# Optimization experiments

Hardware: AMD Instinct MI355X
Metric: run time of the kernel (lower is better)

Reference implementation:

```python
import jax, jax.numpy as jnp
import numpy as np

J = 3
J_H = 5
C_IN = 128
C_OUT = 128
N0, N1, N2 = 1024, 3072, 2048
DENSITY = 0.01
W_SCALE = 0.02  # keeps P^(2^(J_h-1)) @ x @ W magnitudes reasonable in fp32


def _sym_sparse(key, n, density):
    kv, km = jax.random.split(key)
    mask = jax.random.uniform(km, (n, n)) < density
    a = jnp.where(mask, jax.random.normal(kv, (n, n)), 0.0)
    return jnp.triu(a) + jnp.triu(a, 1).T  # symmetric sparse 'Laplacian'


def _sparse(kv, km, shape, density):
    mask = jax.random.uniform(km, shape) < density
    return jnp.where(mask, jax.random.normal(kv, shape), 0.0)


def setup_inputs() -> dict:
    key = jax.random.key(0)
    ks = jax.random.split(key, 24)
    z0 = jax.random.normal(ks[0], (N0, C_IN), jnp.float32)
    z1 = jax.random.normal(ks[1], (N1, C_IN), jnp.float32)
    z2 = jax.random.normal(ks[2], (N2, C_IN), jnp.float32)
    L0 = _sym_sparse(ks[3], N0, 0.02)
    L1_d = _sym_sparse(ks[4], N1, DENSITY)
    L1_u = _sym_sparse(ks[5], N1, DENSITY)
    L2 = _sym_sparse(ks[6], N2, DENSITY)
    B1 = _sparse(ks[7], ks[8], (N0, N1), DENSITY)
    B2 = _sparse(ks[9], ks[10], (N1, N2), DENSITY)
    W_d = jax.random.normal(ks[11], (J, C_IN, C_OUT)) * W_SCALE
    W_u = jax.random.normal(ks[12], (J, C_IN, C_OUT)) * W_SCALE
    W_h = jax.random.normal(ks[13], (C_IN, C_OUT)) * W_SCALE
    W_b1 = jax.random.normal(ks[14], (J, C_IN, C_OUT)) * W_SCALE
    W_b2 = jax.random.normal(ks[15], (J, C_IN, C_OUT)) * W_SCALE
    attn_d_w = jax.random.normal(ks[16], (1, 2 * C_IN)) * W_SCALE
    attn_d_b = jax.random.normal(ks[17], (1,)) * W_SCALE
    attn_u_w = jax.random.normal(ks[18], (1, 2 * C_IN)) * W_SCALE
    attn_u_b = jax.random.normal(ks[19], (1,)) * W_SCALE
    return dict(z0=z0, z1=z1, z2=z2, L0=L0, L1_d=L1_d, L1_u=L1_u, L2=L2,
                B1=B1, B2=B2, W_d=W_d, W_u=W_u, W_h=W_h, W_b1=W_b1, W_b2=W_b2,
                attn_d_w=attn_d_w, attn_d_b=attn_d_b,
                attn_u_w=attn_u_w, attn_u_b=attn_u_b)


def _attention(x, n, w, b, src, dst):
    # gather edge endpoints -> tiny MLP -> sigmoid -> symmetric scatter
    a = jnp.concatenate([x[src], x[dst]], axis=-1)      # [E, 2C]
    s = jax.nn.sigmoid(a @ w.T + b)[:, 0]               # [E]
    return jnp.zeros((n, n), x.dtype).at[src, dst].set(s).at[dst, src].set(s)


def _harmonic(L, x, W_h):
    lmax = jnp.linalg.eigvalsh(L)[-1]
    # torch does lambda_max.item() -> constant w.r.t. grads
    eps = jax.lax.stop_gradient(jnp.where(lmax > 0, 1.0 / lmax, 0.1))
    P = jnp.eye(L.shape[0], dtype=x.dtype) - eps * L
    for _ in range(J_H - 1):
        P = P @ P                                        # P^(2^(J_h-1))
    return P @ x @ W_h


def reference(z0, z1, z2, L0, L1_d, L1_u, L2, B1, B2,
              W_d, W_u, W_h, W_b1, W_b2,
              attn_d_w, attn_d_b, attn_u_w, attn_u_b):
    # nonzero patterns of the Laplacians (constants, computed on host)
    src_d, dst_d = np.nonzero(np.asarray(jax.device_get(L1_d)))
    src_u, dst_u = np.nonzero(np.asarray(jax.device_get(L1_u)))
    L1d_attn = _attention(z1, N1, attn_d_w, attn_d_b,
                          jnp.asarray(src_d), jnp.asarray(dst_d))
    L1u_attn = _attention(z1, N1, attn_u_w, attn_u_b,
                          jnp.asarray(src_u), jnp.asarray(dst_u))
    # sum_j (A @ z) @ W[j] == (A @ z) @ W.sum(0)
    Wd_s, Wu_s = W_d.sum(0), W_u.sum(0)
    Wb1_s, Wb2_s = W_b1.sum(0), W_b2.sum(0)

    z0_out = (L0 @ z0) @ Wd_s + (B1 @ z1) @ Wb1_s + _harmonic(L0, z0, W_h)
    z0_out = jax.nn.relu(z0_out)

    z1_out = ((L1d_attn @ z1) @ Wd_s + (L1u_attn @ z1) @ Wu_s
              + (B1.T @ z0) @ Wb1_s + (B2 @ z2) @ Wb2_s
              + _harmonic(L1_d + L1_u, z1, W_h))
    z1_out = jax.nn.relu(z1_out)

    z2_out = (L2 @ z2) @ Wu_s + (B2.T @ z1) @ Wb2_s + _harmonic(L2, z2, W_h)
    z2_out = jax.nn.relu(z2_out)
    return (z0_out, z1_out, z2_out)
```

## Files before the change

kernel.cpp:

```cpp
#include <hip/hip_runtime.h>
#include <string.h>

constexpr int M_LZ = 48;

constexpr int CAP_L0 = 26240, CAP_L1 = 118016, CAP_L2 = 52480, CAP_B1 = 39360, CAP_B2 = 78720;
constexpr int CB_L0 = 0;
constexpr int CB_L1D = CB_L0 + CAP_L0;
constexpr int CB_L1U = CB_L1D + CAP_L1;
constexpr int CB_L2  = CB_L1U + CAP_L1;
constexpr int CB_B1  = CB_L2 + CAP_L2;
constexpr int CB_B2  = CB_B1 + CAP_B1;
constexpr int CAP_TOT= CB_B2 + CAP_B2;
constexpr int CB_B1T = CAP_TOT;
constexpr int CB_B2T = CB_B1T + CAP_B1;
constexpr int CAP_TOT2 = CB_B2T + CAP_B2;

constexpr int P_L0=0, P_L1D=1025, P_L1U=4098, P_L2=7171, P_B1=9220, P_B2=10245;
constexpr int P_B1T=13320, P_B2T=16393;
constexpr int C_L0=0, C_L1D=1024, C_L1U=4096, C_L2=7168, C_B1=9216, C_B2=10240;
constexpr int C_B1T=13312, C_B2T=16384;

constexpr size_t HBUF  = (size_t)6144*128;

constexpr size_t W_CNT = 0;
constexpr size_t W_PTR = 18432;
constexpr size_t W_CUR = W_PTR + 18444;
constexpr size_t W_CIDX= W_CUR + 5120;
constexpr size_t W_VAL = W_CIDX + CAP_TOT2;
constexpr size_t W_V0  = W_VAL + CAP_TOT2;
constexpr size_t W_PK  = W_V0 + 6144;
constexpr size_t W_TT  = W_PK + (size_t)64*6144*4;
constexpr size_t W_EPS = W_TT + 6144;
constexpr size_t W_UV  = W_EPS + 128;
constexpr size_t W_H   = W_UV + 4*3072;
constexpr size_t W_SCAT= W_H + 15*HBUF;
constexpr size_t S0_OFF= 0;
constexpr size_t S1_OFF= (size_t)1024*384;
constexpr size_t S2_OFF= S1_OFF + (size_t)3072*640;
constexpr size_t SCAT_TOT = S2_OFF + (size_t)2048*384;
constexpr size_t W_WCAT= W_SCAT + SCAT_TOT;
constexpr size_t WC0=0, WC1=(size_t)384*128, WC2=WC1+(size_t)640*128;
constexpr size_t W_SLOT= W_WCAT + (size_t)1408*128;
constexpr size_t W_FLG = W_SLOT + 1048576;
constexpr size_t W_REL = W_FLG + 65536;

__device__ __forceinline__ float wredf(float v){
  #pragma unroll
  for(int o=32;o;o>>=1) v += __shfl_xor(v,o,64);
  return v;
}
__device__ __forceinline__ int wredi(int v){
  #pragma unroll
  for(int o=32;o;o>>=1) v += __shfl_xor(v,o,64);
  return v;
}
__device__ __forceinline__ void red4x2(float4& a0, float4& a1){
  #pragma unroll
  for (int o=16;o<=32;o<<=1){
    a0.x+=__shfl_xor(a0.x,o,64); a0.y+=__shfl_xor(a0.y,o,64);
    a0.z+=__shfl_xor(a0.z,o,64); a0.w+=__shfl_xor(a0.w,o,64);
    a1.x+=__shfl_xor(a1.x,o,64); a1.y+=__shfl_xor(a1.y,o,64);
    a1.z+=__shfl_xor(a1.z,o,64); a1.w+=__shfl_xor(a1.w,o,64);
  }
}
__device__ __forceinline__ float v0hash(int i, float invs){
  unsigned uu=(unsigned)i*2654435761u; uu^=uu>>16; uu*=2246822519u; uu^=uu>>13;
  return (uu&1)?invs:-invs;
}

__device__ __forceinline__ float ldc(const float* p){
  return __hip_atomic_load(p, __ATOMIC_RELAXED, __HIP_MEMORY_SCOPE_AGENT);
}
__device__ __forceinline__ float2 ldc2(const float* p){
  unsigned long long u = __hip_atomic_load((const unsigned long long*)p,
                          __ATOMIC_RELAXED, __HIP_MEMORY_SCOPE_AGENT);
  float2 r; memcpy(&r,&u,8); return r;
}
__device__ __forceinline__ void stc(float* p, float v){
  __hip_atomic_store(p, v, __ATOMIC_RELAXED, __HIP_MEMORY_SCOPE_AGENT);
}
__device__ __forceinline__ void stc2(float* p, float2 v){
  unsigned long long u; memcpy(&u,&v,8);
  __hip_atomic_store((unsigned long long*)p, u, __ATOMIC_RELAXED, __HIP_MEMORY_SCOPE_AGENT);
}
__device__ __forceinline__ int ldci(const int* p){
  return __hip_atomic_load(p, __ATOMIC_RELAXED, __HIP_MEMORY_SCOPE_AGENT);
}
__device__ __forceinline__ void stci(int* p, int v){
  __hip_atomic_store(p, v, __ATOMIC_RELAXED, __HIP_MEMORY_SCOPE_AGENT);
}

__device__ __forceinline__ void barg(float* ws, int* leafs, int b, int lbase, int Ng,
                                     bool chk, int lidx, int ph){
  const int t = threadIdx.x;
  int* flg = (int*)ws + W_FLG;
  __builtin_amdgcn_s_waitcnt(0);
  __syncthreads();
  if (t==0) stci(flg + (size_t)b*32, ph+1);
  if (chk){
    for (int s=t; s<Ng; s+=256){
      const int* f = flg + (size_t)(lbase+s)*32;
      while (ldci(f) < ph+1) __builtin_amdgcn_s_sleep(1);
    }
    __syncthreads();
    if (t==0){
      #pragma unroll
      for (int i=0;i<16;i++) stci(leafs + (size_t)i*32, ph+1);
    }
    __syncthreads();
  } else {
    if (t==0){
      const int* rl = leafs + (size_t)(lidx&15)*32;
      while (ldci(rl) < ph+1) __builtin_amdgcn_s_sleep(1);
    }
    __syncthreads();
  }
}

__device__ __forceinline__ void bar_lz(float* ws, int b, int grp, int lbase, int Lg,
                                       bool chk, int lb, int ph, int j,
                                       float* shr, float* redm,
                                       float& a_o, float& g_o, float& ib_o){
  const int t = threadIdx.x, lane = t&63, wvv = t>>6;
  __builtin_amdgcn_s_waitcnt(0);
  __syncthreads();
  if (t==0){
    float A0=redm[0]+redm[1]+redm[2]+redm[3];
    float G0=redm[4]+redm[5]+redm[6]+redm[7];
    float N0=redm[8]+redm[9]+redm[10]+redm[11];
    float* sl = ws + W_SLOT + ((size_t)j*2048 + b)*8;
    stc2(sl+2, make_float2(A0,G0)); stc(sl+4, N0);
    __builtin_amdgcn_s_waitcnt(0);
    stci((int*)sl, ph+1);
  }
  if (chk){
    float pa=0.f, pg=0.f, pn=0.f;
    for (int s=t; s<Lg; s+=256){
      const float* sl = ws + W_SLOT + ((size_t)j*2048 + lbase+s)*8;
      while (ldci((const int*)sl) < ph+1) __builtin_amdgcn_s_sleep(1);
      float2 ag = ldc2(sl+2); float nn = ldc(sl+4);
      pa+=ag.x; pg+=ag.y; pn+=nn;
    }
    pa=wredf(pa); pg=wredf(pg); pn=wredf(pn);
    if (lane==0){ shr[0*4+wvv]=pa; shr[1*4+wvv]=pg; shr[2*4+wvv]=pn; }
    __syncthreads();
    if (t==0){
      float a=shr[0]+shr[1]+shr[2]+shr[3];
      float g=shr[4]+shr[5]+shr[6]+shr[7];
      float n=shr[8]+shr[9]+shr[10]+shr[11];
      float ib = 1.f/sqrtf(fmaxf(n - a*a - g*g, 1e-20f));
      float* TT = ws + W_TT + (size_t)(grp*64 + j)*32;
      stc2(TT, make_float2(a,g)); stc(TT+2, n);
      #pragma unroll
      for (int i=0;i<16;i++){
        float* lf = ws + W_REL + (size_t)(grp*16+i)*32;
        stc2(lf+2, make_float2(a,g)); stc(lf+4, ib);
      }
      __builtin_amdgcn_s_waitcnt(0);
      #pragma unroll
      for (int i=0;i<16;i++)
        stci((int*)(ws + W_REL) + (size_t)(grp*16+i)*32, ph+1);
      shr[0]=a; shr[1]=g; shr[2]=ib;
    }
    __syncthreads();
  } else {
    if (t==0){
      const float* lf = ws + W_REL + (size_t)(grp*16 + (lb&15))*32;
      while (ldci((const int*)lf) < ph+1) __builtin_amdgcn_s_sleep(1);
      float2 ag = ldc2(lf+2); float ib = ldc(lf+4);
      shr[0]=ag.x; shr[1]=ag.y; shr[2]=ib;
    }
    __syncthreads();
  }
  a_o = shr[0]; g_o = shr[1]; ib_o = shr[2];
}

__global__ void k_wprep(const float* Wd,const float* Wu,const float* Wh,
                        const float* Wb1,const float* Wb2, float* ws){
  int t = blockIdx.x*256 + threadIdx.x;
  if (t >= 16384) return;
  int* wsi = (int*)ws;
  if (t < 5120) wsi[W_CNT + 13312 + t] = 0;
  if (t < 5120) wsi[W_CUR + t] = 0;
  for (int i=t; i<65536+2048; i+=16384) wsi[W_FLG+i] = 0;
  for (int i=t; i<131072; i+=16384) wsi[W_SLOT + (size_t)i*8] = 0;
  float sd = Wd[t]  + Wd[16384+t]  + Wd[32768+t];
  float su = Wu[t]  + Wu[16384+t]  + Wu[32768+t];
  float s1 = Wb1[t] + Wb1[16384+t] + Wb1[32768+t];
  float s2 = Wb2[t] + Wb2[16384+t] + Wb2[32768+t];
  float wh = Wh[t];
  float* W0 = ws + W_WCAT + WC0;
  float* W1 = ws + W_WCAT + WC1;
  float* W2 = ws + W_WCAT + WC2;
  W0[t]=sd; W0[16384+t]=s1; W0[32768+t]=wh;
  W1[t]=sd; W1[16384+t]=su; W1[32768+t]=s1; W1[49152+t]=s2; W1[65536+t]=wh;
  W2[t]=su; W2[16384+t]=s2; W2[32768+t]=wh;
}

__device__ __forceinline__ void mat_meta(int wid, const float* L0,const float* L1d,const float* L1u,
    const float* L2,const float* B1,const float* B2,
    const float*& M,int& ncol,int& lrow,int& co,int& po,int& cb,int& cap,int& tco){
  if (wid < 1024){ M=L0;  ncol=1024; lrow=wid;        co=C_L0;  po=P_L0;  cb=CB_L0;  cap=CAP_L0; tco=-1; }
  else if (wid < 4096){ M=L1d; ncol=3072; lrow=wid-1024;  co=C_L1D; po=P_L1D; cb=CB_L1D; cap=CAP_L1; tco=-1; }
  else if (wid < 7168){ M=L1u; ncol=3072; lrow=wid-4096;  co=C_L1U; po=P_L1U; cb=CB_L1U; cap=CAP_L1; tco=-1; }
  else if (wid < 9216){ M=L2;  ncol=2048; lrow=wid-7168;  co=C_L2;  po=P_L2;  cb=CB_L2;  cap=CAP_L2; tco=-1; }
  else if (wid < 10240){ M=B1; ncol=3072; lrow=wid-9216;  co=C_B1;  po=P_B1;  cb=CB_B1;  cap=CAP_B1; tco=C_B1T; }
  else { M=B2; ncol=2048; lrow=wid-10240; co=C_B2;  po=P_B2;  cb=CB_B2;  cap=CAP_B2; tco=C_B2T; }
}

__global__ void k_count(const float* L0,const float* L1d,const float* L1u,const float* L2,
                        const float* B1,const float* B2,int* cnt){
  int wid = blockIdx.x*4 + (threadIdx.x>>6);
  int lane = threadIdx.x & 63;
  if (wid >= 13312) return;
  const float* M; int ncol,lrow,co,po,cb,cap,tco;
  mat_meta(wid,L0,L1d,L1u,L2,B1,B2,M,ncol,lrow,co,po,cb,cap,tco);
  const float4* row4 = (const float4*)(M + (size_t)lrow*ncol);
  int c = 0;
  for (int j0=0; j0<ncol; j0+=256){
    float4 v = row4[(j0>>2)+lane];
    int n0=v.x!=0.f, n1=v.y!=0.f, n2=v.z!=0.f, n3=v.w!=0.f;
    c += n0+n1+n2+n3;
    if (tco>=0){
      int jb = j0 + lane*4;
      if (n0) atomicAdd(cnt+tco+jb,   1);
      if (n1) atomicAdd(cnt+tco+jb+1, 1);
      if (n2) atomicAdd(cnt+tco+jb+2, 1);
      if (n3) atomicAdd(cnt+tco+jb+3, 1);
    }
  }
  c = wredi(c);
  if (lane==0) cnt[co+lrow] = c;
}

__global__ void k_prefix(const int* cnt, int* ptr, int* cur){
  __shared__ int lds[257];
  const int rows[8]={1024,3072,3072,2048,1024,3072,3072,2048};
  const int cofs[8]={C_L0,C_L1D,C_L1U,C_L2,C_B1,C_B2,C_B1T,C_B2T};
  const int pofs[8]={P_L0,P_L1D,P_L1U,P_L2,P_B1,P_B2,P_B1T,P_B2T};
  int b=blockIdx.x, t=threadIdx.x;
  int R=rows[b]; const int* c=cnt+cofs[b]; int* p=ptr+pofs[b];
  int* cc = (b==6)? cur : (b==7)? cur+3072 : nullptr;
  int chunk=(R+255)/256;
  int lo=t*chunk, hi=min(R,lo+chunk);
  int s=0;
  for(int i=lo;i<hi;i++) s+=c[i];
  lds[t]=s; __syncthreads();
  if(t==0){ int run=0; for(int i=0;i<256;i++){int x=lds[i];lds[i]=run;run+=x;} lds[256]=run; }
  __syncthreads();
  int run=lds[t];
  for(int i=lo;i<hi;i++){ p[i]=run; if(cc) cc[i]=run; run+=c[i]; }
  if(t==0) p[R]=lds[256];
}

__global__ void k_fill(const float* L0,const float* L1d,const float* L1u,const float* L2,
                       const float* B1,const float* B2,const int* ptr,int* cidx,float* val){
  int wid = blockIdx.x*4 + (threadIdx.x>>6);
  int lane = threadIdx.x & 63;
  if (wid >= 13312) return;
  const float* M; int ncol,lrow,co,po,cb,cap,tco;
  mat_meta(wid,L0,L1d,L1u,L2,B1,B2,M,ncol,lrow,co,po,cb,cap,tco);
  const float4* row4 = (const float4*)(M + (size_t)lrow*ncol);
  int base = ptr[po+lrow];
  int run = 0;
  for (int j0=0; j0<ncol; j0+=256){
    float4 v = row4[(j0>>2)+lane];
    int n0=v.x!=0.f, n1=v.y!=0.f, n2=v.z!=0.f, n3=v.w!=0.f;
    int local = n0+n1+n2+n3;
    int incl = local;
    #pragma unroll
    for (int o=1;o<64;o<<=1){
      int tmp = __shfl_up(incl,o,64);
      if (lane>=o) incl += tmp;
    }
    int tot = __shfl(incl,63,64);
    int pos = base + run + incl - local;
    int jb = j0 + lane*4;
    if (n0){ if(pos<cap){cidx[cb+pos]=jb;   val[cb+pos]=v.x;} pos++; }
    if (n1){ if(pos<cap){cidx[cb+pos]=jb+1; val[cb+pos]=v.y;} pos++; }
    if (n2){ if(pos<cap){cidx[cb+pos]=jb+2; val[cb+pos]=v.z;} pos++; }
    if (n3){ if(pos<cap){cidx[cb+pos]=jb+3; val[cb+pos]=v.w;} pos++; }
    run += tot;
  }
}

__global__ void k_fillT(float* ws){
  int wid = blockIdx.x*4 + (threadIdx.x>>6);
  int lane = threadIdx.x & 63;
  if (wid >= 4096) return;
  int* wsi=(int*)ws;
  const int* ptr=wsi+W_PTR; int* cidx=wsi+W_CIDX; float* val=ws+W_VAL;
  int* cur=wsi+W_CUR;
  if (wid < 1024){
    int r=wid;
    int e=ptr[P_B1+r+1];
    for(int k=ptr[P_B1+r]+lane;k<e;k+=64){
      int c=cidx[CB_B1+k]; float v=val[CB_B1+k];
      int pos=atomicAdd(cur+c,1);
      cidx[CB_B1T+pos]=r; val[CB_B1T+pos]=v;
    }
  } else {
    int r=wid-1024;
    int e=ptr[P_B2+r+1];
    for(int k=ptr[P_B2+r]+lane;k<e;k+=64){
      int c=cidx[CB_B2+k]; float v=val[CB_B2+k];
      int pos=atomicAdd(cur+3072+c,1);
      cidx[CB_B2T+pos]=r; val[CB_B2T+pos]=v;
    }
  }
}

__global__ __launch_bounds__(256,8) void k_solve(float* ws,
    const float* z0,const float* z1,const float* z2,
    const float* adw,const float* adb,const float* auw,const float* aub,
    float* out){
  const int b = blockIdx.x, t = threadIdx.x;
  const int wv = t>>6, lane = t&63;
  const int sg = lane>>4, chn = lane&15;
  const int* wsi=(const int*)ws;
  const int* ptr=wsi+W_PTR; const int* cidx=wsi+W_CIDX; const float* val=ws+W_VAL;

  __shared__ float smem[2616];
  float* Sl  = smem;
  float* Wl  = smem + 544;
  float* TTa = smem;
  float* TTb = smem + 64;
  float* redm= smem + 2592;
  float* shr = smem + 2604;

  int* grel = (int*)ws + W_REL + 48*32;
  int* krel = (int*)ws + W_SLOT + 63*2048*8;

  if (b < 768){
    int g, gbase, nb;
    if (b<128){ g=0; gbase=0;   nb=0;    }
    else if (b<512){ g=1; gbase=128; nb=1024; }
    else { g=2; gbase=512; nb=4096; }
    const int lb = b - gbase;
    const int Lg = (g==0)?128:(g==1)?384:256;
    const bool chk = (lb==0);
    const float invsg = (g==0)?0.03125f:(g==1)?0.0180421959f:0.0220970869f;
    const int hw = lane>>5, hl = lane&31;
    const int p  = lb*8 + wv*2 + hw;
    const int gp = nb + p;
    float a=0.f, gmm=0.f, ib=1.f;
    float vp_m1=0.f, vp_m2=0.f, wp_m1=0.f;
    for (int j=0;j<M_LZ;j++){
      float wp=0.f;
      if (j==0){
        #define GZ(PP,CBB) { const int* rp=ptr+PP; int e=rp[p+1]; \
          for (int k=rp[p]+hl;k<e;k+=32){ wp += val[CBB+k]*v0hash(nb+cidx[CBB+k], invsg); } }
        if (g==0){ GZ(P_L0,CB_L0) }
        else if (g==1){ GZ(P_L1D,CB_L1D) GZ(P_L1U,CB_L1U) }
        else { GZ(P_L2,CB_L2) }
        #undef GZ
      } else {
        const float4* pk = (const float4*)(ws + W_PK) + (size_t)(j-1)*6144 + nb;
        #define GP(PP,CBB) { const int* rp=ptr+PP; int e=rp[p+1]; \
          for (int k=rp[p]+hl;k<e;k+=32){ float v=val[CBB+k]; float4 pq=pk[cidx[CBB+k]]; \
            wp += v*((pq.x - a*pq.y - gmm*pq.z)*ib); } }
        if (g==0){ GP(P_L0,CB_L0) }
        else if (g==1){ GP(P_L1D,CB_L1D) GP(P_L1U,CB_L1U) }
        else { GP(P_L2,CB_L2) }
        #undef GP
      }
      #pragma unroll
      for (int o=16;o;o>>=1) wp += __shfl_xor(wp,o,64);
      float rA=0.f, rG=0.f, rN=0.f;
      if (hl==0){
        float vp;
        if (j==0) vp = v0hash(gp, invsg);
        else      vp = (wp_m1 - a*vp_m1 - gmm*vp_m2)*ib;
        float* pkw = ws + W_PK + ((size_t)j*6144 + gp)*4;
        stc2(pkw, make_float2(wp, vp)); stc(pkw+2, vp_m1);
        rA = vp*wp; rG = vp_m1*wp; rN = wp*wp;
        vp_m2 = vp_m1; vp_m1 = vp; wp_m1 = wp;
      }
      rA += __shfl_xor(rA,32,64); rG += __shfl_xor(rG,32,64); rN += __shfl_xor(rN,32,64);
      if (lane==0){ redm[0*4+wv]=rA; redm[1*4+wv]=rG; redm[2*4+wv]=rN; }
      bar_lz(ws, b, g, gbase, Lg, chk, lb, 1+j, j, shr, redm, a, gmm, ib);
    }
    if (chk && t<64){
      int i = t;
      double lo=1e300, hi=-1e300;
      if (i<M_LZ){
        const float* TT = ws + W_TT + (size_t)(g*64 + i)*32;
        float aa=TT[0], gg=TT[1], nn=TT[2];
        TTa[i]=aa; TTb[i]=sqrtf(fmaxf(nn-aa*aa-gg*gg,1e-20f));
      }
      if (i<M_LZ){
        double r=(i? fabs((double)TTb[i-1]):0.0) + (i<M_LZ-1? fabs((double)TTb[i]):0.0);
        lo=(double)TTa[i]-r; hi=(double)TTa[i]+r;
      }
      #pragma unroll
      for(int o=32;o;o>>=1){ lo=fmin(lo,__shfl_xor(lo,o,64)); hi=fmax(hi,__shfl_xor(hi,o,64)); }
      lo -= 1.0; hi += 1.0;
      for (int round=0; round<4; round++){
        double x = lo + (hi-lo)*(double)(i+1)/65.0;
        double d = 1.0; int cnt2=0;
        for (int k2=0;k2<M_LZ;k2++){
          double bi = k2? (double)TTb[k2-1] : 0.0;
          d = ((double)TTa[k2]-x) - bi*bi/d;
          if (d==0.0) d = -1e-300;
          if (d<0.0) cnt2++;
        }
        double nlo = (cnt2< M_LZ)? x : -1e300;
        double nhi = (cnt2==M_LZ)? x :  1e300;
        #pragma unroll
        for(int o=32;o;o>>=1){ nlo=fmax(nlo,__shfl_xor(nlo,o,64)); nhi=fmin(nhi,__shfl_xor(nhi,o,64)); }
        if (nlo>-1e299) lo=nlo;
        if (nhi< 1e299) hi=nhi;
      }
      double lam = 0.5*(lo+hi);
      if (i==0) stc(ws+W_EPS+(size_t)g*32, (lam>0.0)? (float)(1.0/lam) : 0.1f);
    }
  } else {
    const int kb = b - 768;
    const int vw = kb*4 + wv;
    if (vw < 3072){
      float2 x  = ((const float2*)(z1+(size_t)vw*128))[lane];
      float2 a0 = ((const float2*)adw)[lane];
      float2 a1 = ((const float2*)adw)[64+lane];
      float2 b0 = ((const float2*)auw)[lane];
      float2 b1 = ((const float2*)auw)[64+lane];
      float ud=x.x*a0.x+x.y*a0.y, vd=x.x*a1.x+x.y*a1.y;
      float uu=x.x*b0.x+x.y*b0.y, vu=x.x*b1.x+x.y*b1.y;
      ud=wredf(ud); vd=wredf(vd); uu=wredf(uu); vu=wredf(vu);
      if(lane==0){ stc(ws+W_UV+vw,ud); stc(ws+W_UV+3072+vw,vd);
                   stc(ws+W_UV+6144+vw,uu); stc(ws+W_UV+9216+vw,vu); }
    }
    int cgP, nbP, lrP; float e0P;
    if (vw < 3072){ cgP=1; nbP=1024; lrP=vw;      e0P=(1.f/28.f); }
    else          { cgP=2; nbP=4096; lrP=vw-3072; e0P=0.0625f;    }
    const bool has2 = (vw >= 4096);
    const int lr2 = vw - 4096;
    for (int k2=1; k2<=16; k2++){
      const float* ybase = ws + W_H + (size_t)(k2>=2? k2-2:0)*HBUF;
      #define KG2(PP,CBB,NBV,ZZV,LRV) { const int* rp=ptr+PP; int e=rp[(LRV)+1]; \
        for (int kk=rp[LRV]+sg; kk<e; kk+=4){ \
          float v=val[CBB+kk]; int q=cidx[CBB+kk]; \
          const float* sr = (k2==1)? (ZZV)+(size_t)q*128 : ybase+(size_t)((NBV)+q)*128; \
          float4 x0=((const float4*)sr)[chn*2], x1=((const float4*)sr)[chn*2+1]; \
          a0.x+=v*x0.x; a0.y+=v*x0.y; a0.z+=v*x0.z; a0.w+=v*x0.w; \
          a1.x+=v*x1.x; a1.y+=v*x1.y; a1.z+=v*x1.z; a1.w+=v*x1.w; \
        } }
      #define KWRITE(CGV,LRV,GRV,E0V) if (lane<16){ \
          float* dst; \
          if (k2<16) dst = ws + W_H + (size_t)(k2-1)*HBUF + (size_t)(GRV)*128; \
          else { \
            if ((CGV)==0)      dst = ws+W_SCAT+S0_OFF+256 + (size_t)(LRV)*384; \
            else if ((CGV)==1) dst = ws+W_SCAT+S1_OFF+512 + (size_t)(LRV)*640; \
            else               dst = ws+W_SCAT+S2_OFF+256 + (size_t)(LRV)*384; \
          } \
          stc2(dst+chn*8,   make_float2((E0V)*a0.x, (E0V)*a0.y)); \
          stc2(dst+chn*8+2, make_float2((E0V)*a0.z, (E0V)*a0.w)); \
          stc2(dst+chn*8+4, make_float2((E0V)*a1.x, (E0V)*a1.y)); \
          stc2(dst+chn*8+6, make_float2((E0V)*a1.z, (E0V)*a1.w)); }
      {
        float4 a0={0.f,0.f,0.f,0.f}, a1={0.f,0.f,0.f,0.f};
        if (cgP==1){ KG2(P_L1D,CB_L1D,1024,z1,lrP) KG2(P_L1U,CB_L1U,1024,z1,lrP) }
        else { KG2(P_L2,CB_L2,4096,z2,lrP) }
        red4x2(a0,a1);
        KWRITE(cgP, lrP, nbP+lrP, e0P)
      }
      if (has2){
        float4 a0={0.f,0.f,0.f,0.f}, a1={0.f,0.f,0.f,0.f};
        KG2(P_L0,CB_L0,0,z0,lr2)
        red4x2(a0,a1);
        KWRITE(0, lr2, lr2, 0.0625f)
      }
      #undef KG2
      #undef KWRITE
      if (k2<16) barg(ws, krel, b, 768, 1280, b==768, kb, k2);
    }
    for (int wid2 = kb*4+wv; wid2 < 18432; wid2 += 5120){
      int task,p2;
      if(wid2<1024){task=0;p2=wid2;}
      else if(wid2<2048){task=1;p2=wid2-1024;}
      else if(wid2<5120){task=2;p2=wid2-2048;}
      else if(wid2<8192){task=3;p2=wid2-5120;}
      else if(wid2<11264){task=4;p2=wid2-8192;}
      else if(wid2<13312){task=5;p2=wid2-11264;}
      else if(wid2<16384){task=6;p2=wid2-13312;}
      else {task=7;p2=wid2-16384;}
      const float* in; const int* rp; int cb2; float* outp; int ostride;
      int mode=0; float Vp=0.f, bb=0.f; const float* U=nullptr;
      switch(task){
        case 0: rp=ptr+P_L0;  cb2=CB_L0;  in=z0; outp=ws+W_SCAT+S0_OFF+0;   ostride=384; break;
        case 1: rp=ptr+P_B1;  cb2=CB_B1;  in=z1; outp=ws+W_SCAT+S0_OFF+128; ostride=384; break;
        case 2: rp=ptr+P_L1D; cb2=CB_L1D; in=z1; outp=ws+W_SCAT+S1_OFF+0;   ostride=640;
                mode=1; U=ws+W_UV; Vp=ws[W_UV+3072+p2]; bb=adb[0]; break;
        case 3: rp=ptr+P_L1U; cb2=CB_L1U; in=z1; outp=ws+W_SCAT+S1_OFF+128; ostride=640;
                mode=1; U=ws+W_UV+6144; Vp=ws[W_UV+9216+p2]; bb=aub[0]; break;
        case 4: rp=ptr+P_B2;  cb2=CB_B2;  in=z2; outp=ws+W_SCAT+S1_OFF+384; ostride=640; break;
        case 5: rp=ptr+P_L2;  cb2=CB_L2;  in=z2; outp=ws+W_SCAT+S2_OFF+0;   ostride=384; break;
        case 6: rp=ptr+P_B1T; cb2=CB_B1T; in=z0; outp=ws+W_SCAT+S1_OFF+256; ostride=640; break;
        default:rp=ptr+P_B2T; cb2=CB_B2T; in=z1; outp=ws+W_SCAT+S2_OFF+128; ostride=384; break;
      }
      float4 a0={0.f,0.f,0.f,0.f}, a1={0.f,0.f,0.f,0.f};
      int e=rp[p2+1];
      for (int k=rp[p2]+sg; k<e; k+=4){
        int q = cidx[cb2+k];
        float v;
        if (mode) v = 1.0f/(1.0f+__expf(-(U[q]+Vp+bb)));
        else v = val[cb2+k];
        const float* sr = in + (size_t)q*128;
        float4 x0 = ((const float4*)sr)[chn*2];
        float4 x1 = ((const float4*)sr)[chn*2+1];
        a0.x+=v*x0.x; a0.y+=v*x0.y; a0.z+=v*x0.z; a0.w+=v*x0.w;
        a1.x+=v*x1.x; a1.y+=v*x1.y; a1.z+=v*x1.z; a1.w+=v*x1.w;
      }
      red4x2(a0, a1);
      if (sg==0){
        float* dst = outp + (size_t)p2*ostride;
        stc2(dst+chn*8,   make_float2(a0.x,a0.y));
        stc2(dst+chn*8+2, make_float2(a0.z,a0.w));
        stc2(dst+chn*8+4, make_float2(a1.x,a1.y));
        stc2(dst+chn*8+6, make_float2(a1.z,a1.w));
      }
    }
  }

  barg(ws, grel, b, 0, 2048, b==1, b, 30);

  { int r = b*4+wv;
    if (r < 6144){
      int cg = (r<1024)?0:(r<4096)?1:2;
      int lr = r - ((cg==0)?0:(cg==1)?1024:4096);
      const float* zz = (cg==0)?z0:(cg==1)?z1:z2;
      float lam0 = (cg==1)?28.f:16.f;
      float eps  = ws[W_EPS+(size_t)cg*32];
      float rr = eps*lam0;
      float* hc;
      if (cg==0)      hc = ws+W_SCAT+S0_OFF+256 + (size_t)lr*384;
      else if (cg==1) hc = ws+W_SCAT+S1_OFF+512 + (size_t)lr*640;
      else            hc = ws+W_SCAT+S2_OFF+256 + (size_t)lr*384;
      const float BIN[17] = {1.f,16.f,120.f,560.f,1820.f,4368.f,8008.f,11440.f,12870.f,
                             11440.f,8008.f,4368.f,1820.f,560.f,120.f,16.f,1.f};
      float2 acc = ((const float2*)(zz + (size_t)lr*128))[lane];
      float rk = 1.f;
      #pragma unroll
      for (int k2=1;k2<=15;k2++){
        rk *= -rr;
        float2 y = ((const float2*)(ws + W_H + (size_t)(k2-1)*HBUF + (size_t)r*128))[lane];
        float c = BIN[k2]*rk;
        acc.x += c*y.x; acc.y += c*y.y;
      }
      rk *= -rr;
      float2 y16 = ((const float2*)hc)[lane];
      acc.x += rk*y16.x; acc.y += rk*y16.y;
      stc2(hc + (size_t)lane*2, acc);
    }
  }
  barg(ws, grel, b, 0, 2048, b==1, b, 31);

  if (b < 192){
    const float* S; const float* W; float* outp; int K; int blk;
    if (b<32){       S=ws+W_SCAT+S0_OFF; W=ws+W_WCAT+WC0; outp=out;        K=384; blk=b; }
    else if (b<128){ S=ws+W_SCAT+S1_OFF; W=ws+W_WCAT+WC1; outp=out+131072; K=640; blk=b-32; }
    else {           S=ws+W_SCAT+S2_OFF; W=ws+W_WCAT+WC2; outp=out+524288; K=384; blk=b-128; }
    int r0=blk*32;
    int ty=t>>5, tx=t&31;
    float acc[4][4]={};
    for (int k0=0; k0<K; k0+=16){
      {
        int r=t>>3, kq=(t&7)*2;
        const float* src=S+(size_t)(r0+r)*K + k0+kq;
        Sl[r*17+kq]=src[0]; Sl[r*17+kq+1]=src[1];
      }
      {
        int kk=t>>4, cq=(t&15)*8;
        const float* src=W+(size_t)(k0+kk)*128+cq;
        #pragma unroll
        for(int i=0;i<8;i++) Wl[kk*128+cq+i]=src[i];
      }
      __syncthreads();
      #pragma unroll
      for(int k=0;k<16;k++){
        float sv[4], wvv2[4];
        #pragma unroll
        for(int i=0;i<4;i++) sv[i]=Sl[(ty*4+i)*17+k];
        #pragma unroll
        for(int i=0;i<4;i++) wvv2[i]=Wl[k*128+tx+32*i];
        #pragma unroll
        for(int a2=0;a2<4;a2++)
          #pragma unroll
          for(int b2=0;b2<4;b2++) acc[a2][b2]+=sv[a2]*wvv2[b2];
      }
      __syncthreads();
    }
    #pragma unroll
    for(int a2=0;a2<4;a2++)
      #pragma unroll
      for(int b2=0;b2<4;b2++){
        int r=r0+ty*4+a2, col=tx+32*b2;
        outp[(size_t)r*128+col]=fmaxf(acc[a2][b2],0.f);
      }
  }
}

extern "C" void kernel_launch(void* const* d_in, const int* in_sizes, int n_in,
                              void* d_out, int out_size, void* d_ws, size_t ws_size,
                              hipStream_t stream){
  const float* z0 =(const float*)d_in[0];
  const float* z1 =(const float*)d_in[1];
  const float* z2 =(const float*)d_in[2];
  const float* L0 =(const float*)d_in[3];
  const float* L1d=(const float*)d_in[4];
  const float* L1u=(const float*)d_in[5];
  const float* L2 =(const float*)d_in[6];
  const float* B1 =(const float*)d_in[7];
  const float* B2 =(const float*)d_in[8];
  const float* Wd =(const float*)d_in[9];
  const float* Wu =(const float*)d_in[10];
  const float* Wh =(const float*)d_in[11];
  const float* Wb1=(const float*)d_in[12];
  const float* Wb2=(const float*)d_in[13];
  const float* adw=(const float*)d_in[14];
  const float* adb=(const float*)d_in[15];
  const float* auw=(const float*)d_in[16];
  const float* aub=(const float*)d_in[17];
  float* ws=(float*)d_ws;
  int* wsi=(int*)d_ws;
  float* out=(float*)d_out;

  hipLaunchKernelGGL(k_wprep, dim3(64), dim3(256), 0, stream, Wd,Wu,Wh,Wb1,Wb2,ws);
  hipLaunchKernelGGL(k_count, dim3(3328), dim3(256), 0, stream, L0,L1d,L1u,L2,B1,B2, wsi+W_CNT);
  hipLaunchKernelGGL(k_prefix, dim3(8), dim3(256), 0, stream, wsi+W_CNT, wsi+W_PTR, wsi+W_CUR);
  hipLaunchKernelGGL(k_fill, dim3(3328), dim3(256), 0, stream, L0,L1d,L1u,L2,B1,B2, wsi+W_PTR, wsi+W_CIDX, ws+W_VAL);
  hipLaunchKernelGGL(k_fillT, dim3(1024), dim3(256), 0, stream, ws);
  hipLaunchKernelGGL(k_solve, dim3(2048), dim3(256), 0, stream,
                     ws, z0, z1, z2, adw, adb, auw, aub, out);
}
```

Before: 780.1 us.

## Fuse CSR build kernels into persistent solve kernel with grid barriers

The count, prefix, fill and transpose-fill kernels are folded into the single persistent solve kernel, separated by grid-wide barriers. The transpose fill is moved into the blocks that previously only waited during the Lanczos phase, so it overlaps that work. The intent is to remove four kernel launches and their inter-kernel gaps. In exchange the stages depend on software grid barriers, and many loads and stores become cache-bypassing so that data written before a barrier is visible across blocks.

```diff
diff --git a/kernel.cpp b/kernel.cpp
--- a/kernel.cpp
+++ b/kernel.cpp
@@ -180,8 +180,8 @@
   int t = blockIdx.x*256 + threadIdx.x;
   if (t >= 16384) return;
   int* wsi = (int*)ws;
-  if (t < 5120) wsi[W_CNT + 13312 + t] = 0;
-  if (t < 5120) wsi[W_CUR + t] = 0;
+  if (t < 5120) stci(wsi + W_CNT + 13312 + t, 0);
+  if (t < 5120) stci(wsi + W_CUR + t, 0);
   for (int i=t; i<65536+2048; i+=16384) wsi[W_FLG+i] = 0;
   for (int i=t; i<131072; i+=16384) wsi[W_SLOT + (size_t)i*8] = 0;
   float sd = Wd[t]  + Wd[16384+t]  + Wd[32768+t];
@@ -208,117 +208,18 @@
   else { M=B2; ncol=2048; lrow=wid-10240; co=C_B2;  po=P_B2;  cb=CB_B2;  cap=CAP_B2; tco=C_B2T; }
 }
 
-__global__ void k_count(const float* L0,const float* L1d,const float* L1u,const float* L2,
-                        const float* B1,const float* B2,int* cnt){
-  int wid = blockIdx.x*4 + (threadIdx.x>>6);
-  int lane = threadIdx.x & 63;
-  if (wid >= 13312) return;
-  const float* M; int ncol,lrow,co,po,cb,cap,tco;
-  mat_meta(wid,L0,L1d,L1u,L2,B1,B2,M,ncol,lrow,co,po,cb,cap,tco);
-  const float4* row4 = (const float4*)(M + (size_t)lrow*ncol);
-  int c = 0;
-  for (int j0=0; j0<ncol; j0+=256){
-    float4 v = row4[(j0>>2)+lane];
-    int n0=v.x!=0.f, n1=v.y!=0.f, n2=v.z!=0.f, n3=v.w!=0.f;
-    c += n0+n1+n2+n3;
-    if (tco>=0){
-      int jb = j0 + lane*4;
-      if (n0) atomicAdd(cnt+tco+jb,   1);
-      if (n1) atomicAdd(cnt+tco+jb+1, 1);
-      if (n2) atomicAdd(cnt+tco+jb+2, 1);
-      if (n3) atomicAdd(cnt+tco+jb+3, 1);
-    }
-  }
-  c = wredi(c);
-  if (lane==0) cnt[co+lrow] = c;
-}
-
-__global__ void k_prefix(const int* cnt, int* ptr, int* cur){
-  __shared__ int lds[257];
-  const int rows[8]={1024,3072,3072,2048,1024,3072,3072,2048};
-  const int cofs[8]={C_L0,C_L1D,C_L1U,C_L2,C_B1,C_B2,C_B1T,C_B2T};
-  const int pofs[8]={P_L0,P_L1D,P_L1U,P_L2,P_B1,P_B2,P_B1T,P_B2T};
-  int b=blockIdx.x, t=threadIdx.x;
-  int R=rows[b]; const int* c=cnt+cofs[b]; int* p=ptr+pofs[b];
-  int* cc = (b==6)? cur : (b==7)? cur+3072 : nullptr;
-  int chunk=(R+255)/256;
-  int lo=t*chunk, hi=min(R,lo+chunk);
-  int s=0;
-  for(int i=lo;i<hi;i++) s+=c[i];
-  lds[t]=s; __syncthreads();
-  if(t==0){ int run=0; for(int i=0;i<256;i++){int x=lds[i];lds[i]=run;run+=x;} lds[256]=run; }
-  __syncthreads();
-  int run=lds[t];
-  for(int i=lo;i<hi;i++){ p[i]=run; if(cc) cc[i]=run; run+=c[i]; }
-  if(t==0) p[R]=lds[256];
-}
-
-__global__ void k_fill(const float* L0,const float* L1d,const float* L1u,const float* L2,
-                       const float* B1,const float* B2,const int* ptr,int* cidx,float* val){
-  int wid = blockIdx.x*4 + (threadIdx.x>>6);
-  int lane = threadIdx.x & 63;
-  if (wid >= 13312) return;
-  const float* M; int ncol,lrow,co,po,cb,cap,tco;
-  mat_meta(wid,L0,L1d,L1u,L2,B1,B2,M,ncol,lrow,co,po,cb,cap,tco);
-  const float4* row4 = (const float4*)(M + (size_t)lrow*ncol);
-  int base = ptr[po+lrow];
-  int run = 0;
-  for (int j0=0; j0<ncol; j0+=256){
-    float4 v = row4[(j0>>2)+lane];
-    int n0=v.x!=0.f, n1=v.y!=0.f, n2=v.z!=0.f, n3=v.w!=0.f;
-    int local = n0+n1+n2+n3;
-    int incl = local;
-    #pragma unroll
-    for (int o=1;o<64;o<<=1){
-      int tmp = __shfl_up(incl,o,64);
-      if (lane>=o) incl += tmp;
-    }
-    int tot = __shfl(incl,63,64);
-    int pos = base + run + incl - local;
-    int jb = j0 + lane*4;
-    if (n0){ if(pos<cap){cidx[cb+pos]=jb;   val[cb+pos]=v.x;} pos++; }
-    if (n1){ if(pos<cap){cidx[cb+pos]=jb+1; val[cb+pos]=v.y;} pos++; }
-    if (n2){ if(pos<cap){cidx[cb+pos]=jb+2; val[cb+pos]=v.z;} pos++; }
-    if (n3){ if(pos<cap){cidx[cb+pos]=jb+3; val[cb+pos]=v.w;} pos++; }
-    run += tot;
-  }
-}
-
-__global__ void k_fillT(float* ws){
-  int wid = blockIdx.x*4 + (threadIdx.x>>6);
-  int lane = threadIdx.x & 63;
-  if (wid >= 4096) return;
-  int* wsi=(int*)ws;
-  const int* ptr=wsi+W_PTR; int* cidx=wsi+W_CIDX; float* val=ws+W_VAL;
-  int* cur=wsi+W_CUR;
-  if (wid < 1024){
-    int r=wid;
-    int e=ptr[P_B1+r+1];
-    for(int k=ptr[P_B1+r]+lane;k<e;k+=64){
-      int c=cidx[CB_B1+k]; float v=val[CB_B1+k];
-      int pos=atomicAdd(cur+c,1);
-      cidx[CB_B1T+pos]=r; val[CB_B1T+pos]=v;
-    }
-  } else {
-    int r=wid-1024;
-    int e=ptr[P_B2+r+1];
-    for(int k=ptr[P_B2+r]+lane;k<e;k+=64){
-      int c=cidx[CB_B2+k]; float v=val[CB_B2+k];
-      int pos=atomicAdd(cur+3072+c,1);
-      cidx[CB_B2T+pos]=r; val[CB_B2T+pos]=v;
-    }
-  }
-}
-
-__global__ __launch_bounds__(256,8) void k_solve(float* ws,
+__global__ __launch_bounds__(256,8) void k_all(float* ws,
     const float* z0,const float* z1,const float* z2,
+    const float* L0,const float* L1d,const float* L1u,
+    const float* L2,const float* B1,const float* B2,
     const float* adw,const float* adb,const float* auw,const float* aub,
     float* out){
   const int b = blockIdx.x, t = threadIdx.x;
   const int wv = t>>6, lane = t&63;
   const int sg = lane>>4, chn = lane&15;
-  const int* wsi=(const int*)ws;
-  const int* ptr=wsi+W_PTR; const int* cidx=wsi+W_CIDX; const float* val=ws+W_VAL;
+  int* wsi=(int*)ws;
+  int* ptrm=wsi+W_PTR; int* cnm=wsi+W_CNT;
+  int* cidxm=wsi+W_CIDX; float* valm=ws+W_VAL;
 
   __shared__ float smem[2616];
   float* Sl  = smem;
@@ -330,6 +231,78 @@
 
   int* grel = (int*)ws + W_REL + 48*32;
   int* krel = (int*)ws + W_SLOT + 63*2048*8;
+
+  for (int wid = b*4+wv; wid < 13312; wid += 8192){
+    const float* M; int ncol,lrow,co,po,cb,cap,tco;
+    mat_meta(wid,L0,L1d,L1u,L2,B1,B2,M,ncol,lrow,co,po,cb,cap,tco);
+    const float4* row4 = (const float4*)(M + (size_t)lrow*ncol);
+    int c = 0;
+    for (int j0=0; j0<ncol; j0+=256){
+      float4 v = row4[(j0>>2)+lane];
+      int n0=v.x!=0.f, n1=v.y!=0.f, n2=v.z!=0.f, n3=v.w!=0.f;
+      c += n0+n1+n2+n3;
+      if (tco>=0){
+        int jb = j0 + lane*4;
+        if (n0) atomicAdd(cnm+tco+jb,   1);
+        if (n1) atomicAdd(cnm+tco+jb+1, 1);
+        if (n2) atomicAdd(cnm+tco+jb+2, 1);
+        if (n3) atomicAdd(cnm+tco+jb+3, 1);
+      }
+    }
+    c = wredi(c);
+    if (lane==0) stci(cnm+co+lrow, c);
+  }
+  barg(ws, grel, b, 0, 2048, b==0, b, 0);
+
+  if (b < 8){
+    int* lds = (int*)smem;
+    const int rows[8]={1024,3072,3072,2048,1024,3072,3072,2048};
+    const int cofs[8]={C_L0,C_L1D,C_L1U,C_L2,C_B1,C_B2,C_B1T,C_B2T};
+    const int pofs[8]={P_L0,P_L1D,P_L1U,P_L2,P_B1,P_B2,P_B1T,P_B2T};
+    int R=rows[b]; const int* c=cnm+cofs[b]; int* p=ptrm+pofs[b];
+    int* cc = (b==6)? (wsi+W_CUR) : (b==7)? (wsi+W_CUR+3072) : nullptr;
+    int chunk=(R+255)/256;
+    int lo=t*chunk, hi=min(R,lo+chunk);
+    int s=0;
+    for(int i=lo;i<hi;i++) s+=ldci(c+i);
+    lds[t]=(float)0, ((int*)lds)[t]=s; __syncthreads();
+    if(t==0){ int run=0; for(int i=0;i<256;i++){int x=((int*)lds)[i];((int*)lds)[i]=run;run+=x;} ((int*)lds)[256]=run; }
+    __syncthreads();
+    int run=((int*)lds)[t];
+    for(int i=lo;i<hi;i++){ stci(p+i, run); if(cc) stci(cc+i, run); run+=ldci(c+i); }
+    if(t==0) stci(p+R, ((int*)lds)[256]);
+  }
+  barg(ws, grel, b, 0, 2048, b==0, b, 1);
+
+  for (int wid = b*4+wv; wid < 13312; wid += 8192){
+    const float* M; int ncol,lrow,co,po,cb,cap,tco;
+    mat_meta(wid,L0,L1d,L1u,L2,B1,B2,M,ncol,lrow,co,po,cb,cap,tco);
+    const float4* row4 = (const float4*)(M + (size_t)lrow*ncol);
+    int base = ldci(ptrm+po+lrow);
+    int run = 0;
+    for (int j0=0; j0<ncol; j0+=256){
+      float4 v = row4[(j0>>2)+lane];
+      int n0=v.x!=0.f, n1=v.y!=0.f, n2=v.z!=0.f, n3=v.w!=0.f;
+      int local = n0+n1+n2+n3;
+      int incl = local;
+      #pragma unroll
+      for (int o=1;o<64;o<<=1){
+        int tmp = __shfl_up(incl,o,64);
+        if (lane>=o) incl += tmp;
+      }
+      int tot = __shfl(incl,63,64);
+      int pos = base + run + incl - local;
+      int jb = j0 + lane*4;
+      if (n0){ if(pos<cap){stci(cidxm+cb+pos,jb);   stc(valm+cb+pos,v.x);} pos++; }
+      if (n1){ if(pos<cap){stci(cidxm+cb+pos,jb+1); stc(valm+cb+pos,v.y);} pos++; }
+      if (n2){ if(pos<cap){stci(cidxm+cb+pos,jb+2); stc(valm+cb+pos,v.z);} pos++; }
+      if (n3){ if(pos<cap){stci(cidxm+cb+pos,jb+3); stc(valm+cb+pos,v.w);} pos++; }
+      run += tot;
+    }
+  }
+  barg(ws, grel, b, 0, 2048, b==0, b, 2);
+
+  const int* ptr=ptrm; const int* cidx=cidxm; const float* val=valm;
 
   if (b < 768){
     int g, gbase, nb;
@@ -385,7 +358,7 @@
       double lo=1e300, hi=-1e300;
       if (i<M_LZ){
         const float* TT = ws + W_TT + (size_t)(g*64 + i)*32;
-        float aa=TT[0], gg=TT[1], nn=TT[2];
+        float aa=ldc(TT), gg=ldc(TT+1), nn=ldc(TT+2);
         TTa[i]=aa; TTb[i]=sqrtf(fmaxf(nn-aa*aa-gg*gg,1e-20f));
       }
       if (i<M_LZ){
@@ -415,6 +388,28 @@
       if (i==0) stc(ws+W_EPS+(size_t)g*32, (lam>0.0)? (float)(1.0/lam) : 0.1f);
     }
   } else {
+    { int widT = (b-768)*4+wv;
+      if (widT < 4096){
+        int* cur=wsi+W_CUR;
+        if (widT < 1024){
+          int r=widT;
+          int s0=ldci(ptr+P_B1+r); int e=ldci(ptr+P_B1+r+1);
+          for(int k=s0+lane;k<e;k+=64){
+            int c=ldci(cidx+CB_B1+k); float v=ldc(val+CB_B1+k);
+            int pos=atomicAdd(cur+c,1);
+            stci(cidxm+CB_B1T+pos,r); stc(valm+CB_B1T+pos,v);
+          }
+        } else {
+          int r=widT-1024;
+          int s0=ldci(ptr+P_B2+r); int e=ldci(ptr+P_B2+r+1);
+          for(int k=s0+lane;k<e;k+=64){
+            int c=ldci(cidx+CB_B2+k); float v=ldc(val+CB_B2+k);
+            int pos=atomicAdd(cur+3072+c,1);
+            stci(cidxm+CB_B2T+pos,r); stc(valm+CB_B2T+pos,v);
+          }
+        }
+      }
+    }
     const int kb = b - 768;
     const int vw = kb*4 + wv;
     if (vw < 3072){
@@ -471,7 +466,7 @@
       }
       #undef KG2
       #undef KWRITE
-      if (k2<16) barg(ws, krel, b, 768, 1280, b==768, kb, k2);
+      if (k2<16) barg(ws, krel, b, 768, 1280, b==768, kb, k2+3);
     }
     for (int wid2 = kb*4+wv; wid2 < 18432; wid2 += 5120){
       int task,p2;
@@ -489,9 +484,9 @@
         case 0: rp=ptr+P_L0;  cb2=CB_L0;  in=z0; outp=ws+W_SCAT+S0_OFF+0;   ostride=384; break;
         case 1: rp=ptr+P_B1;  cb2=CB_B1;  in=z1; outp=ws+W_SCAT+S0_OFF+128; ostride=384; break;
         case 2: rp=ptr+P_L1D; cb2=CB_L1D; in=z1; outp=ws+W_SCAT+S1_OFF+0;   ostride=640;
-                mode=1; U=ws+W_UV; Vp=ws[W_UV+3072+p2]; bb=adb[0]; break;
+                mode=1; U=ws+W_UV; Vp=ldc(ws+W_UV+3072+p2); bb=adb[0]; break;
         case 3: rp=ptr+P_L1U; cb2=CB_L1U; in=z1; outp=ws+W_SCAT+S1_OFF+128; ostride=640;
-                mode=1; U=ws+W_UV+6144; Vp=ws[W_UV+9216+p2]; bb=aub[0]; break;
+                mode=1; U=ws+W_UV+6144; Vp=ldc(ws+W_UV+9216+p2); bb=aub[0]; break;
         case 4: rp=ptr+P_B2;  cb2=CB_B2;  in=z2; outp=ws+W_SCAT+S1_OFF+384; ostride=640; break;
         case 5: rp=ptr+P_L2;  cb2=CB_L2;  in=z2; outp=ws+W_SCAT+S2_OFF+0;   ostride=384; break;
         case 6: rp=ptr+P_B1T; cb2=CB_B1T; in=z0; outp=ws+W_SCAT+S1_OFF+256; ostride=640; break;
@@ -502,7 +497,7 @@
       for (int k=rp[p2]+sg; k<e; k+=4){
         int q = cidx[cb2+k];
         float v;
-        if (mode) v = 1.0f/(1.0f+__expf(-(U[q]+Vp+bb)));
+        if (mode) v = 1.0f/(1.0f+__expf(-(ldc(U+q)+Vp+bb)));
         else v = val[cb2+k];
         const float* sr = in + (size_t)q*128;
         float4 x0 = ((const float4*)sr)[chn*2];
@@ -529,7 +524,7 @@
       int lr = r - ((cg==0)?0:(cg==1)?1024:4096);
       const float* zz = (cg==0)?z0:(cg==1)?z1:z2;
       float lam0 = (cg==1)?28.f:16.f;
-      float eps  = ws[W_EPS+(size_t)cg*32];
+      float eps  = ldc(ws+W_EPS+(size_t)cg*32);
       float rr = eps*lam0;
       float* hc;
       if (cg==0)      hc = ws+W_SCAT+S0_OFF+256 + (size_t)lr*384;
@@ -621,14 +616,10 @@
   const float* auw=(const float*)d_in[16];
   const float* aub=(const float*)d_in[17];
   float* ws=(float*)d_ws;
-  int* wsi=(int*)d_ws;
   float* out=(float*)d_out;
 
   hipLaunchKernelGGL(k_wprep, dim3(64), dim3(256), 0, stream, Wd,Wu,Wh,Wb1,Wb2,ws);
-  hipLaunchKernelGGL(k_count, dim3(3328), dim3(256), 0, stream, L0,L1d,L1u,L2,B1,B2, wsi+W_CNT);
-  hipLaunchKernelGGL(k_prefix, dim3(8), dim3(256), 0, stream, wsi+W_CNT, wsi+W_PTR, wsi+W_CUR);
-  hipLaunchKernelGGL(k_fill, dim3(3328), dim3(256), 0, stream, L0,L1d,L1u,L2,B1,B2, wsi+W_PTR, wsi+W_CIDX, ws+W_VAL);
-  hipLaunchKernelGGL(k_fillT, dim3(1024), dim3(256), 0, stream, ws);
-  hipLaunchKernelGGL(k_solve, dim3(2048), dim3(256), 0, stream,
-                     ws, z0, z1, z2, adw, adb, auw, aub, out);
-}
+  hipLaunchKernelGGL(k_all, dim3(2048), dim3(256), 0, stream,
+                     ws, z0, z1, z2, L0, L1d, L1u, L2, B1, B2,
+                     adw, adb, auw, aub, out);
+}
```

After: 804.3 us. 1.03x slower.
